# Performance work log

Hardware: AMD Instinct MI355X
Metric: run time of the kernel (lower is better)

The kernel has to match this reference:

```python
import jax, jax.numpy as jnp
import numpy as np

THRESHOLD = 0.5     # overlap_thresh
NEG_POS = 3         # negative:positive ratio
VAR = (0.1, 0.2)    # cfg['variance']


def point_form(pr):
    # cxcywh -> xmin,ymin,xmax,ymax
    return jnp.concatenate([pr[:, :2] - pr[:, 2:] / 2, pr[:, :2] + pr[:, 2:] / 2], axis=1)


def jaccard(a, b):
    # a: [N,4] point-form truths, b: [P,4] point-form priors -> IoU [N,P]
    lt = jnp.maximum(a[:, None, :2], b[None, :, :2])
    rb = jnp.minimum(a[:, None, 2:], b[None, :, 2:])
    wh = jnp.clip(rb - lt, 0.0)
    inter = wh[..., 0] * wh[..., 1]
    area_a = ((a[:, 2] - a[:, 0]) * (a[:, 3] - a[:, 1]))[:, None]
    area_b = ((b[:, 2] - b[:, 0]) * (b[:, 3] - b[:, 1]))[None, :]
    return inter / (area_a + area_b - inter)


def encode(matched, priors):
    # matched: [P,4] point-form, priors: [P,4] cxcywh
    g_cxcy = ((matched[:, :2] + matched[:, 2:]) / 2 - priors[:, :2]) / (VAR[0] * priors[:, 2:])
    g_wh = jnp.log((matched[:, 2:] - matched[:, :2]) / priors[:, 2:]) / VAR[1]
    return jnp.concatenate([g_cxcy, g_wh], axis=1)


def match_one(truths, labels, priors):
    # truths [N,4], labels [N], priors [P,4] cxcywh
    N = truths.shape[0]
    P = priors.shape[0]
    overlaps = jaccard(truths, point_form(priors))          # [N,P]
    best_prior_idx = jnp.argmax(overlaps, axis=1)           # [N] best prior per truth
    best_truth_overlap = jnp.max(overlaps, axis=0)          # [P]
    best_truth_idx = jnp.argmax(overlaps, axis=0)           # [P]
    # ensure each truth's best prior is kept (overlap forced to 2)
    best_truth_overlap = best_truth_overlap.at[best_prior_idx].set(2.0)
    hit = best_prior_idx[:, None] == jnp.arange(P)[None, :]  # [N,P]
    chosen = jnp.max(jnp.where(hit, jnp.arange(N)[:, None], -1), axis=0)
    best_truth_idx = jnp.where(chosen >= 0, chosen, best_truth_idx)
    matched = truths[best_truth_idx]                        # [P,4]
    conf = labels[best_truth_idx].astype(jnp.int32) + 1
    conf = jnp.where(best_truth_overlap < THRESHOLD, 0, conf)
    return encode(matched, priors), conf


def smooth_l1(x):
    ax = jnp.abs(x)
    return jnp.where(ax < 1.0, 0.5 * ax * ax, ax - 0.5)


def multibox_loss(loc_data, conf_data, priors, targets):
    num, P, C = conf_data.shape
    truths = targets[..., :4]
    labels = targets[..., 4]
    loc_t, conf_t = jax.vmap(match_one, in_axes=(0, 0, None))(truths, labels, priors)
    pos = conf_t > 0                                        # [B,P]

    # localization loss over positives
    loss_l = jnp.sum(jnp.where(pos[..., None], smooth_l1(loc_data - loc_t), 0.0))

    # hard-negative mining score: logsumexp - conf[label clamped to {0,1}]
    batch_conf = jax.lax.stop_gradient(conf_data).reshape(-1, C)
    conf_flat = conf_t.reshape(-1)
    clamped = jnp.where(conf_flat != 0, 1, conf_flat)
    # replicate torch nonzero()-indexing quirk: row 0 also set to 1 if any positive exists
    clamped = clamped.at[0].set(jnp.where(jnp.any(conf_flat != 0), 1, clamped[0]))
    lse = jax.scipy.special.logsumexp(batch_conf, axis=1)
    loss_c = lse - jnp.take_along_axis(batch_conf, clamped[:, None], axis=1)[:, 0]
    loss_c = loss_c.reshape(num, P)
    loss_c = jnp.where(pos, 0.0, loss_c)
    # rank of each prior by descending mining loss
    idx_rank = jnp.argsort(jnp.argsort(-loss_c, axis=1), axis=1)
    num_pos = jnp.sum(pos.astype(jnp.int32), axis=1, keepdims=True)  # [B,1]
    num_neg = jnp.clip(NEG_POS * num_pos, None, P - 1)
    neg = idx_rank < num_neg
    sel = pos | neg

    # confidence cross-entropy over selected priors, original labels as targets
    logp = jax.nn.log_softmax(conf_data, axis=-1)           # [B,P,C]
    ce = -jnp.take_along_axis(logp, conf_t[..., None], axis=-1)[..., 0]
    loss_conf = jnp.sum(jnp.where(sel, ce, 0.0))

    Nf = jnp.sum(num_pos).astype(jnp.float32)
    return loss_l / Nf, loss_conf / Nf


def setup_inputs() -> dict:
    key = jax.random.key(0)
    k1, k2, k3, k4, k5, k6, k7 = jax.random.split(key, 7)
    B, P, C, NOBJ = 128, 8732, 21, 20
    loc_data = jax.random.normal(k1, (B, P, 4), jnp.float32)
    conf_data = jax.random.normal(k2, (B, P, C), jnp.float32)
    pcxy = jax.random.uniform(k3, (P, 2), jnp.float32, 0.05, 0.95)
    pwh = jax.random.uniform(k4, (P, 2), jnp.float32, 0.05, 0.4)
    priors = jnp.concatenate([pcxy, pwh], axis=1)           # cxcywh
    mins = jax.random.uniform(k5, (B, NOBJ, 2), jnp.float32, 0.0, 0.6)
    wh = jax.random.uniform(k6, (B, NOBJ, 2), jnp.float32, 0.05, 0.35)
    lab = jax.random.randint(k7, (B, NOBJ), 0, C - 1).astype(jnp.float32)
    targets = jnp.concatenate([mins, mins + wh, lab[..., None]], axis=-1)
    return {"loc_data": loc_data, "conf_data": conf_data, "priors": priors, "targets": targets}


def reference(loc_data, conf_data, priors, targets):
    return multibox_loss(loc_data, conf_data, priors, targets)
```

## Files before the change

kernel.cpp:

```cpp
#include <hip/hip_runtime.h>

#define PP 8732
#define NB 20
#define NC 21
#define BTH 256
#define NCH 35
#define BTS 1024
#define NWS (BTS/64)

__device__ __forceinline__ float sl1(float d){
  float a = fabsf(d);
  return a < 1.0f ? 0.5f*a*a : a - 0.5f;
}

__device__ __forceinline__ float wave_max64(float x){
  int t;
  t = __builtin_amdgcn_update_dpp(0, __float_as_int(x), 0x111, 0xF, 0xF, true); x = fmaxf(x, __int_as_float(t));
  t = __builtin_amdgcn_update_dpp(0, __float_as_int(x), 0x112, 0xF, 0xF, true); x = fmaxf(x, __int_as_float(t));
  t = __builtin_amdgcn_update_dpp(0, __float_as_int(x), 0x114, 0xF, 0xF, true); x = fmaxf(x, __int_as_float(t));
  t = __builtin_amdgcn_update_dpp(0, __float_as_int(x), 0x118, 0xF, 0xF, true); x = fmaxf(x, __int_as_float(t));
  t = __builtin_amdgcn_update_dpp(0, __float_as_int(x), 0x142, 0xF, 0xF, true); x = fmaxf(x, __int_as_float(t));
  t = __builtin_amdgcn_update_dpp(0, __float_as_int(x), 0x143, 0xF, 0xF, true); x = fmaxf(x, __int_as_float(t));
  return __int_as_float(__builtin_amdgcn_readlane(__float_as_int(x), 63));
}

__device__ __forceinline__ int wave_sum64_lane63(int x){
  x += __builtin_amdgcn_update_dpp(0, x, 0x111, 0xF, 0xF, true);
  x += __builtin_amdgcn_update_dpp(0, x, 0x112, 0xF, 0xF, true);
  x += __builtin_amdgcn_update_dpp(0, x, 0x114, 0xF, 0xF, true);
  x += __builtin_amdgcn_update_dpp(0, x, 0x118, 0xF, 0xF, true);
  x += __builtin_amdgcn_update_dpp(0, x, 0x142, 0xF, 0xF, true);
  x += __builtin_amdgcn_update_dpp(0, x, 0x143, 0xF, 0xF, true);
  return x;
}

extern "C" __global__ void __launch_bounds__(BTH)
mb_main(const float* __restrict__ conf_data,
        const float* __restrict__ priors,
        const float* __restrict__ targets,
        float* __restrict__ rankneg,
        unsigned char* __restrict__ meta,
        unsigned long long* __restrict__ keys2)
{
  const int b = blockIdx.x, chunk = blockIdx.y;
  const int tid = threadIdx.x, lane = tid & 63, wid = tid >> 6;
  const int q0 = chunk*BTH + wid*64;
  const int cnt = (q0 < PP) ? ((PP - q0 < 64) ? (PP - q0) : 64) : 0;

  __shared__ __align__(16) float s_buf[4][64*NC];
  __shared__ unsigned long long s_keys[4][NB];

  const bool valid = (lane < cnt);
  const int p  = q0 + lane;
  const int pl = valid ? p : 0;

  float tx=0.f, ty=0.f, tz=0.f, tw=0.f;
  if (lane < NB){
    const float* tp = targets + ((long)b*NB + lane)*5;
    tx = tp[0]; ty = tp[1]; tz = tp[2]; tw = tp[3];
  }
  float4 pr = reinterpret_cast<const float4*>(priors)[pl];

  if (cnt == 64){
    const char* g = (const char*)(conf_data + ((long)b*PP + q0)*NC) + lane*16;
    char* l0 = (char*)&s_buf[wid][0];
    #pragma unroll
    for (int i=0;i<5;i++)
      __builtin_amdgcn_global_load_lds(
        (const __attribute__((address_space(1))) void*)(g + i*1024),
        (__attribute__((address_space(3))) void*)(l0 + i*1024), 16, 0, 0);
    if (lane < 16)
      __builtin_amdgcn_global_load_lds(
        (const __attribute__((address_space(1))) void*)(g + 5*1024),
        (__attribute__((address_space(3))) void*)(l0 + 5*1024), 16, 0, 0);
  } else if (cnt > 0){
    const float4* cb4 = reinterpret_cast<const float4*>(conf_data + ((long)b*PP + q0)*NC);
    float4* sb4 = reinterpret_cast<float4*>(s_buf[wid]);
    const int tot4 = (cnt*NC) >> 2;
    for (int i=lane; i<tot4; i+=64) sb4[i] = cb4[i];
  }

  float bx1 = pr.x - pr.z*0.5f, by1 = pr.y - pr.w*0.5f;
  float bx2 = pr.x + pr.z*0.5f, by2 = pr.y + pr.w*0.5f;
  float area_b = (bx2-bx1)*(by2-by1);
  float area_a = (tz-tx)*(tw-ty);
  float bestov = -1.0f; int bestn = 0;
  unsigned long long mykey = 0ULL;

  if (cnt > 0){
    #pragma unroll 4
    for (int n=0;n<NB;n++){
      float t_x = __int_as_float(__builtin_amdgcn_readlane(__float_as_int(tx), n));
      float t_y = __int_as_float(__builtin_amdgcn_readlane(__float_as_int(ty), n));
      float t_z = __int_as_float(__builtin_amdgcn_readlane(__float_as_int(tz), n));
      float t_w = __int_as_float(__builtin_amdgcn_readlane(__float_as_int(tw), n));
      float aa  = __int_as_float(__builtin_amdgcn_readlane(__float_as_int(area_a), n));
      float lx=fmaxf(t_x,bx1), ly=fmaxf(t_y,by1);
      float rx=fminf(t_z,bx2), ry=fminf(t_w,by2);
      float iw=fmaxf(rx-lx,0.f), ih=fmaxf(ry-ly,0.f);
      float inter = iw*ih;
      float iou = inter * __builtin_amdgcn_rcpf(aa + area_b - inter);
      if (iou > bestov){ bestov=iou; bestn=n; }

      float iouv = valid ? iou : -1.0f;
      float wmax = wave_max64(iouv);
      unsigned long long mk = __ballot(valid && (iou == wmax));
      int wlane = __ffsll((long long)mk) - 1;
      unsigned long long key = ((unsigned long long)__float_as_uint(wmax)<<32)
                             | (unsigned long long)(0xFFFFFFFFu - (unsigned)(q0 + wlane));
      if (lane == n) mykey = key;
    }
  }
  if (lane < NB) s_keys[wid][lane] = mykey;

  if (cnt > 0){
    asm volatile("s_waitcnt vmcnt(0)" ::: "memory");

    const float* v = s_buf[wid] + lane*NC;
    float vv[NC];
    #pragma unroll
    for (int c=0;c<NC;c++) vv[c] = v[c];
    float m = vv[0];
    #pragma unroll
    for (int c=1;c<NC;c++) m = fmaxf(m, vv[c]);
    float s = 0.f;
    #pragma unroll
    for (int c=0;c<NC;c++) s += __expf(vv[c]-m);
    float lse = __logf(s) + m;
    if (valid){
      rankneg[(long)b*PP + p] = lse - vv[0];
      meta[(long)b*PP + p] = (unsigned char)((bestn<<1) | (bestov >= 0.5f ? 1 : 0));
    }
  }

  __syncthreads();
  if (tid < NB){
    unsigned long long mx = s_keys[0][tid];
    #pragma unroll
    for (int w=1;w<4;w++) if (s_keys[w][tid] > mx) mx = s_keys[w][tid];
    keys2[((long)b*NCH + chunk)*NB + tid] = mx;
  }
}

extern "C" __global__ void __launch_bounds__(BTS)
mb_select(const float* __restrict__ loc_data,
          const float* __restrict__ conf_data,
          const float* __restrict__ priors,
          const float* __restrict__ targets,
          const float* __restrict__ rankneg,
          const unsigned char* __restrict__ meta,
          const unsigned long long* __restrict__ keys2,
          float* __restrict__ rowres, int* __restrict__ ticket,
          float* __restrict__ out, int Bn)
{
  const int b = blockIdx.x, tid = threadIdx.x, lane = tid & 63, wid = tid >> 6;
  __shared__ __align__(16) float s_val[PP];
  __shared__ __align__(16) unsigned int s_meta4[PP/4];
  __shared__ float4 s_tr4[NB];
  __shared__ float s_lab[NB];
  __shared__ int   s_bp[NB];
  __shared__ int   s_tot[32];
  __shared__ float s_fa[NWS], s_fb[NWS], s_fc[NWS];
  __shared__ int   s_ia[NWS];
  __shared__ float s_rowll, s_rowpc;
  __shared__ int   s_npos, s_last;
  unsigned char* s_meta = (unsigned char*)s_meta4;
  float4* sv4 = reinterpret_cast<float4*>(s_val);

  const float4* rr = reinterpret_cast<const float4*>(rankneg + (long)b*PP);
  for (int i=tid;i<PP/4;i+=BTS) sv4[i]=rr[i];
  const unsigned int* mr = reinterpret_cast<const unsigned int*>(meta + (long)b*PP);
  for (int i=tid;i<PP/4;i+=BTS) s_meta4[i]=mr[i];
  if (tid < NB*5){
    int n = tid/5, k2 = tid-n*5;
    float vv = targets[((long)b*NB+n)*5+k2];
    if (k2<4) ((float*)&s_tr4[n])[k2]=vv; else s_lab[n]=vv;
  }
  if (tid < NB){
    unsigned long long mx = 0ULL;
    #pragma unroll
    for (int c=0;c<NCH;c++){
      unsigned long long kk = keys2[((long)b*NCH + c)*NB + tid];
      if (kk > mx) mx = kk;
    }
    s_bp[tid] = (int)(0xFFFFFFFFu - (unsigned)(mx & 0xFFFFFFFFULL));
  }
  if (tid < 32) s_tot[tid] = 0;
  __syncthreads();

  if (tid==0){
    for (int n=0;n<NB;n++) s_meta[s_bp[n]] = (unsigned char)((n<<1)|1);
  }
  __syncthreads();

  float4 rv0 = sv4[tid];
  float4 rv1 = sv4[tid+1024];
  float4 rv2 = (tid < PP/4-2048) ? sv4[tid+2048]
                                 : make_float4(0.f,0.f,0.f,0.f);
  unsigned mm0 = s_meta4[tid];
  unsigned mm1 = s_meta4[tid+1024];
  unsigned mm2 = (tid < PP/4-2048) ? s_meta4[tid+2048] : 0u;
  if (mm0 & 0x00000001u) rv0.x = 0.f;
  if (mm0 & 0x00000100u) rv0.y = 0.f;
  if (mm0 & 0x00010000u) rv0.z = 0.f;
  if (mm0 & 0x01000000u) rv0.w = 0.f;
  if (mm1 & 0x00000001u) rv1.x = 0.f;
  if (mm1 & 0x00000100u) rv1.y = 0.f;
  if (mm1 & 0x00010000u) rv1.z = 0.f;
  if (mm1 & 0x01000000u) rv1.w = 0.f;
  if (mm2 & 0x00000001u) rv2.x = 0.f;
  if (mm2 & 0x00000100u) rv2.y = 0.f;
  if (mm2 & 0x00010000u) rv2.z = 0.f;
  if (mm2 & 0x01000000u) rv2.w = 0.f;

  int spec = 0; float delta = 0.f, val0 = 0.f;
  if (b==0 && tid==0 && !(mm0 & 1u)){
    float v0 = conf_data[0], v1 = conf_data[1];
    float r0 = rv0.x;
    float r0p = r0 + v0 - v1;
    delta = r0 - r0p;
    spec = 1;
    rv0.x = r0p; val0 = r0p;
  }

  float ll=0.f, pc=0.f; int np=0;
  for (int p=tid;p<PP;p+=BTS){
    int mt = s_meta[p];
    if (mt & 1){
      np++;
      int n = mt>>1;
      int ct = (int)s_lab[n] + 1;
      const float* cp = conf_data + ((long)b*PP+p)*NC;
      float v0 = cp[0], vct = cp[ct];
      pc += s_val[p] + v0 - vct;
      float4 t = s_tr4[n];
      float4 prr = reinterpret_cast<const float4*>(priors)[p];
      float4 ld = reinterpret_cast<const float4*>(loc_data)[(long)b*PP+p];
      float g0 = ((t.x+t.z)*0.5f - prr.x)/(0.1f*prr.z);
      float g1 = ((t.y+t.w)*0.5f - prr.y)/(0.1f*prr.w);
      float g2 = __logf((t.z-t.x)/prr.z)/0.2f;
      float g3 = __logf((t.w-t.y)/prr.w)/0.2f;
      ll += sl1(ld.x-g0)+sl1(ld.y-g1)+sl1(ld.z-g2)+sl1(ld.w-g3);
    }
  }
  #pragma unroll
  for (int o=32;o;o>>=1){
    ll += __shfl_down(ll,o,64);
    pc += __shfl_down(pc,o,64);
    np += __shfl_down(np,o,64);
  }
  if (lane==0){ s_fa[wid]=ll; s_fb[wid]=pc; s_ia[wid]=np; }
  __syncthreads();
  if (tid==0){
    float a=0.f,c2=0.f; int ni=0;
    for (int w=0;w<NWS;w++){ a+=s_fa[w]; c2+=s_fb[w]; ni+=s_ia[w]; }
    s_rowll=a; s_rowpc=c2; s_npos=ni;
  }
  __syncthreads();
  const int num_pos = s_npos;
  int k = num_pos*3; if (k > PP-1) k = PP-1;

  float negsum = 0.f;
  if (k > 0){
    unsigned lo=0u, hi=0x7f800000u;
    int it=0;
    while (lo < hi){
      unsigned mid = lo + ((hi - lo + 1u) >> 1);
      int c = (__float_as_uint(rv0.x)>=mid) + (__float_as_uint(rv0.y)>=mid)
            + (__float_as_uint(rv0.z)>=mid) + (__float_as_uint(rv0.w)>=mid)
            + (__float_as_uint(rv1.x)>=mid) + (__float_as_uint(rv1.y)>=mid)
            + (__float_as_uint(rv1.z)>=mid) + (__float_as_uint(rv1.w)>=mid)
            + (__float_as_uint(rv2.x)>=mid) + (__float_as_uint(rv2.y)>=mid)
            + (__float_as_uint(rv2.z)>=mid) + (__float_as_uint(rv2.w)>=mid);
      c = wave_sum64_lane63(c);
      if (lane==63) atomicAdd(&s_tot[it], c);
      __syncthreads();
      int tot = s_tot[it];
      if (tot >= k) lo = mid; else hi = mid - 1u;
      it++;
    }
    const unsigned vstar = lo;

    int cg=0; float sg=0.f;
    #define ACC(x) if (__float_as_uint(x)>vstar){cg++;sg+=(x);}
    ACC(rv0.x) ACC(rv0.y) ACC(rv0.z) ACC(rv0.w)
    ACC(rv1.x) ACC(rv1.y) ACC(rv1.z) ACC(rv1.w)
    ACC(rv2.x) ACC(rv2.y) ACC(rv2.z) ACC(rv2.w)
    #undef ACC
    #pragma unroll
    for (int o=32;o;o>>=1){ cg += __shfl_down(cg,o,64); sg += __shfl_down(sg,o,64); }
    __syncthreads();
    if (lane==0){ s_ia[wid]=cg; s_fa[wid]=sg; }
    __syncthreads();
    if (tid==0){
      int cG=0; float sumG=0.f;
      for (int w=0;w<NWS;w++){ cG+=s_ia[w]; sumG+=s_fa[w]; }
      int tie = k - cG;
      negsum = sumG + (float)tie * __uint_as_float(vstar);
      if (b==0 && spec && __float_as_uint(val0) >= vstar) negsum += delta;
    }
  }

  if (tid==0){
    rowres[b*4+0] = s_rowll;
    rowres[b*4+1] = s_rowpc + negsum;
    rowres[b*4+2] = (float)num_pos;
    __threadfence();
    int t = atomicAdd(ticket, 1);
    s_last = (t == gridDim.x - 1) ? 1 : 0;
  }
  __syncthreads();

  if (s_last){
    __threadfence();
    float a0=0.f, a1=0.f, a2=0.f;
    for (int i=tid;i<Bn;i+=BTS){
      a0 += rowres[i*4+0]; a1 += rowres[i*4+1]; a2 += rowres[i*4+2];
    }
    #pragma unroll
    for (int o=32;o;o>>=1){
      a0 += __shfl_down(a0,o,64);
      a1 += __shfl_down(a1,o,64);
      a2 += __shfl_down(a2,o,64);
    }
    if (lane==0){ s_fa[wid]=a0; s_fb[wid]=a1; s_fc[wid]=a2; }
    __syncthreads();
    if (tid==0){
      float A0=0.f,A1=0.f,A2=0.f;
      for (int w=0;w<NWS;w++){ A0+=s_fa[w]; A1+=s_fb[w]; A2+=s_fc[w]; }
      out[0] = A0/A2;
      out[1] = A1/A2;
    }
  }
}

extern "C" void kernel_launch(void* const* d_in, const int* in_sizes, int n_in,
                              void* d_out, int out_size, void* d_ws, size_t ws_size,
                              hipStream_t stream) {
  const float* loc     = (const float*)d_in[0];
  const float* conf    = (const float*)d_in[1];
  const float* priors  = (const float*)d_in[2];
  const float* targets = (const float*)d_in[3];
  float* out = (float*)d_out;
  int B = in_sizes[0] / (PP*4);

  char* ws = (char*)d_ws;
  int*   ticket = (int*)ws;
  float* rowres = (float*)(ws + 64);
  unsigned long long* keys2 = (unsigned long long*)(ws + 4096);
  size_t off_rank = 4096 + (size_t)B*NCH*NB*8;
  float* rankneg = (float*)(ws + off_rank);
  unsigned char* metaa = (unsigned char*)(ws + off_rank + (size_t)B*PP*4);

  hipMemsetAsync(d_ws, 0, 64, stream);
  hipLaunchKernelGGL(mb_main,   dim3(B, NCH), dim3(BTH), 0, stream,
                     conf, priors, targets, rankneg, metaa, keys2);
  hipLaunchKernelGGL(mb_select, dim3(B), dim3(BTS), 0, stream,
                     loc, conf, priors, targets, rankneg, metaa, keys2,
                     rowres, ticket, out, B);
}
```

Before: 202.1 us.

## Fuse main and select kernels using per-row last-block ticket

Merges the two kernels into one launch with 1024-thread blocks over 9 chunks per row. The last chunk block to finish each row, detected through a per-row atomic counter, runs the hard-negative selection and loss reduction, which removes the second launch and its tail. Confidence rows are now loaded directly into registers as float4 instead of through LDS async copies, and rankneg is read from global memory instead of being staged in shared memory. In exchange, only one block per row does the selection work while the other blocks exit, and the larger blocks may lower occupancy in the first phase.

```diff
diff --git a/kernel.cpp b/kernel.cpp
--- a/kernel.cpp
+++ b/kernel.cpp
@@ -3,10 +3,9 @@
 #define PP 8732
 #define NB 20
 #define NC 21
-#define BTH 256
-#define NCH 35
 #define BTS 1024
-#define NWS (BTS/64)
+#define NWS 16
+#define NCH 9
 
 __device__ __forceinline__ float sl1(float d){
   float a = fabsf(d);
@@ -34,60 +33,60 @@
   return x;
 }
 
-extern "C" __global__ void __launch_bounds__(BTH)
-mb_main(const float* __restrict__ conf_data,
-        const float* __restrict__ priors,
-        const float* __restrict__ targets,
-        float* __restrict__ rankneg,
-        unsigned char* __restrict__ meta,
-        unsigned long long* __restrict__ keys2)
+extern "C" __global__ void __launch_bounds__(BTS)
+mb_fused(const float* __restrict__ loc_data,
+         const float* __restrict__ conf_data,
+         const float* __restrict__ priors,
+         const float* __restrict__ targets,
+         float* __restrict__ rankneg,
+         unsigned char* __restrict__ meta,
+         unsigned long long* __restrict__ keys2,
+         int* __restrict__ done,
+         float* __restrict__ rowres, int* __restrict__ ticket,
+         float* __restrict__ out, int Bn)
 {
   const int b = blockIdx.x, chunk = blockIdx.y;
   const int tid = threadIdx.x, lane = tid & 63, wid = tid >> 6;
-  const int q0 = chunk*BTH + wid*64;
+  const int q0 = chunk*BTS + wid*64;
   const int cnt = (q0 < PP) ? ((PP - q0 < 64) ? (PP - q0) : 64) : 0;
 
-  __shared__ __align__(16) float s_buf[4][64*NC];
-  __shared__ unsigned long long s_keys[4][NB];
-
-  const bool valid = (lane < cnt);
-  const int p  = q0 + lane;
-  const int pl = valid ? p : 0;
-
-  float tx=0.f, ty=0.f, tz=0.f, tw=0.f;
-  if (lane < NB){
-    const float* tp = targets + ((long)b*NB + lane)*5;
-    tx = tp[0]; ty = tp[1]; tz = tp[2]; tw = tp[3];
-  }
-  float4 pr = reinterpret_cast<const float4*>(priors)[pl];
-
-  if (cnt == 64){
-    const char* g = (const char*)(conf_data + ((long)b*PP + q0)*NC) + lane*16;
-    char* l0 = (char*)&s_buf[wid][0];
-    #pragma unroll
-    for (int i=0;i<5;i++)
-      __builtin_amdgcn_global_load_lds(
-        (const __attribute__((address_space(1))) void*)(g + i*1024),
-        (__attribute__((address_space(3))) void*)(l0 + i*1024), 16, 0, 0);
-    if (lane < 16)
-      __builtin_amdgcn_global_load_lds(
-        (const __attribute__((address_space(1))) void*)(g + 5*1024),
-        (__attribute__((address_space(3))) void*)(l0 + 5*1024), 16, 0, 0);
-  } else if (cnt > 0){
-    const float4* cb4 = reinterpret_cast<const float4*>(conf_data + ((long)b*PP + q0)*NC);
-    float4* sb4 = reinterpret_cast<float4*>(s_buf[wid]);
-    const int tot4 = (cnt*NC) >> 2;
-    for (int i=lane; i<tot4; i+=64) sb4[i] = cb4[i];
-  }
-
-  float bx1 = pr.x - pr.z*0.5f, by1 = pr.y - pr.w*0.5f;
-  float bx2 = pr.x + pr.z*0.5f, by2 = pr.y + pr.w*0.5f;
-  float area_b = (bx2-bx1)*(by2-by1);
-  float area_a = (tz-tx)*(tw-ty);
-  float bestov = -1.0f; int bestn = 0;
+  __shared__ unsigned long long s_keys[NWS][NB];
+  __shared__ __align__(16) unsigned int s_meta4[PP/4];
+  __shared__ float4 s_tr4[NB];
+  __shared__ float s_lab[NB];
+  __shared__ int   s_bp[NB];
+  __shared__ int   s_tot[32];
+  __shared__ float s_fa[NWS], s_fb[NWS], s_fc[NWS];
+  __shared__ int   s_ia[NWS];
+  __shared__ float s_rowll, s_rowpc;
+  __shared__ int   s_npos, s_go, s_last;
+  unsigned char* s_meta = (unsigned char*)s_meta4;
+
   unsigned long long mykey = 0ULL;
 
   if (cnt > 0){
+    const bool valid = (lane < cnt);
+    const int p  = q0 + lane;
+    const int pl = valid ? p : q0;
+
+    float tx=0.f, ty=0.f, tz=0.f, tw=0.f;
+    if (lane < NB){
+      const float* tp = targets + ((long)b*NB + lane)*5;
+      tx = tp[0]; ty = tp[1]; tz = tp[2]; tw = tp[3];
+    }
+    float4 pr = reinterpret_cast<const float4*>(priors)[pl];
+
+    const float* cb = conf_data + ((long)b*PP + pl)*NC;
+    const float4* cb4 = reinterpret_cast<const float4*>(cb);
+    float4 ca0 = cb4[0], ca1 = cb4[1], ca2 = cb4[2], ca3 = cb4[3], ca4 = cb4[4];
+    float c20 = cb[20];
+
+    float bx1 = pr.x - pr.z*0.5f, by1 = pr.y - pr.w*0.5f;
+    float bx2 = pr.x + pr.z*0.5f, by2 = pr.y + pr.w*0.5f;
+    float area_b = (bx2-bx1)*(by2-by1);
+    float area_a = (tz-tx)*(tw-ty);
+    float bestov = -1.0f; int bestn = 0;
+
     #pragma unroll 4
     for (int n=0;n<NB;n++){
       float t_x = __int_as_float(__builtin_amdgcn_readlane(__float_as_int(tx), n));
@@ -110,16 +109,10 @@
                              | (unsigned long long)(0xFFFFFFFFu - (unsigned)(q0 + wlane));
       if (lane == n) mykey = key;
     }
-  }
-  if (lane < NB) s_keys[wid][lane] = mykey;
-
-  if (cnt > 0){
-    asm volatile("s_waitcnt vmcnt(0)" ::: "memory");
-
-    const float* v = s_buf[wid] + lane*NC;
-    float vv[NC];
-    #pragma unroll
-    for (int c=0;c<NC;c++) vv[c] = v[c];
+
+    float vv[NC] = {ca0.x,ca0.y,ca0.z,ca0.w, ca1.x,ca1.y,ca1.z,ca1.w,
+                    ca2.x,ca2.y,ca2.z,ca2.w, ca3.x,ca3.y,ca3.z,ca3.w,
+                    ca4.x,ca4.y,ca4.z,ca4.w, c20};
     float m = vv[0];
     #pragma unroll
     for (int c=1;c<NC;c++) m = fmaxf(m, vv[c]);
@@ -132,49 +125,35 @@
       meta[(long)b*PP + p] = (unsigned char)((bestn<<1) | (bestov >= 0.5f ? 1 : 0));
     }
   }
+  if (lane < NB) s_keys[wid][lane] = mykey;
 
   __syncthreads();
   if (tid < NB){
     unsigned long long mx = s_keys[0][tid];
     #pragma unroll
-    for (int w=1;w<4;w++) if (s_keys[w][tid] > mx) mx = s_keys[w][tid];
+    for (int w=1;w<NWS;w++) if (s_keys[w][tid] > mx) mx = s_keys[w][tid];
     keys2[((long)b*NCH + chunk)*NB + tid] = mx;
   }
-}
-
-extern "C" __global__ void __launch_bounds__(BTS)
-mb_select(const float* __restrict__ loc_data,
-          const float* __restrict__ conf_data,
-          const float* __restrict__ priors,
-          const float* __restrict__ targets,
-          const float* __restrict__ rankneg,
-          const unsigned char* __restrict__ meta,
-          const unsigned long long* __restrict__ keys2,
-          float* __restrict__ rowres, int* __restrict__ ticket,
-          float* __restrict__ out, int Bn)
-{
-  const int b = blockIdx.x, tid = threadIdx.x, lane = tid & 63, wid = tid >> 6;
-  __shared__ __align__(16) float s_val[PP];
-  __shared__ __align__(16) unsigned int s_meta4[PP/4];
-  __shared__ float4 s_tr4[NB];
-  __shared__ float s_lab[NB];
-  __shared__ int   s_bp[NB];
-  __shared__ int   s_tot[32];
-  __shared__ float s_fa[NWS], s_fb[NWS], s_fc[NWS];
-  __shared__ int   s_ia[NWS];
-  __shared__ float s_rowll, s_rowpc;
-  __shared__ int   s_npos, s_last;
-  unsigned char* s_meta = (unsigned char*)s_meta4;
-  float4* sv4 = reinterpret_cast<float4*>(s_val);
+
+  __threadfence();
+  __syncthreads();
+  if (tid == 0) s_go = (atomicAdd(&done[b], 1) == NCH-1) ? 1 : 0;
+  __syncthreads();
+  if (!s_go) return;
+
+  __threadfence();
 
   const float4* rr = reinterpret_cast<const float4*>(rankneg + (long)b*PP);
-  for (int i=tid;i<PP/4;i+=BTS) sv4[i]=rr[i];
+  float4 rv0 = rr[tid];
+  float4 rv1 = rr[tid+1024];
+  float4 rv2 = (tid < PP/4-2048) ? rr[tid+2048] : make_float4(0.f,0.f,0.f,0.f);
+
   const unsigned int* mr = reinterpret_cast<const unsigned int*>(meta + (long)b*PP);
   for (int i=tid;i<PP/4;i+=BTS) s_meta4[i]=mr[i];
   if (tid < NB*5){
     int n = tid/5, k2 = tid-n*5;
-    float vv = targets[((long)b*NB+n)*5+k2];
-    if (k2<4) ((float*)&s_tr4[n])[k2]=vv; else s_lab[n]=vv;
+    float vvv = targets[((long)b*NB+n)*5+k2];
+    if (k2<4) ((float*)&s_tr4[n])[k2]=vvv; else s_lab[n]=vvv;
   }
   if (tid < NB){
     unsigned long long mx = 0ULL;
@@ -193,10 +172,6 @@
   }
   __syncthreads();
 
-  float4 rv0 = sv4[tid];
-  float4 rv1 = sv4[tid+1024];
-  float4 rv2 = (tid < PP/4-2048) ? sv4[tid+2048]
-                                 : make_float4(0.f,0.f,0.f,0.f);
   unsigned mm0 = s_meta4[tid];
   unsigned mm1 = s_meta4[tid+1024];
   unsigned mm2 = (tid < PP/4-2048) ? s_meta4[tid+2048] : 0u;
@@ -232,7 +207,7 @@
       int ct = (int)s_lab[n] + 1;
       const float* cp = conf_data + ((long)b*PP+p)*NC;
       float v0 = cp[0], vct = cp[ct];
-      pc += s_val[p] + v0 - vct;
+      pc += rankneg[(long)b*PP + p] + v0 - vct;
       float4 t = s_tr4[n];
       float4 prr = reinterpret_cast<const float4*>(priors)[p];
       float4 ld = reinterpret_cast<const float4*>(loc_data)[(long)b*PP+p];
@@ -307,7 +282,7 @@
     rowres[b*4+2] = (float)num_pos;
     __threadfence();
     int t = atomicAdd(ticket, 1);
-    s_last = (t == gridDim.x - 1) ? 1 : 0;
+    s_last = (t == Bn - 1) ? 1 : 0;
   }
   __syncthreads();
 
@@ -346,16 +321,16 @@
 
   char* ws = (char*)d_ws;
   int*   ticket = (int*)ws;
-  float* rowres = (float*)(ws + 64);
-  unsigned long long* keys2 = (unsigned long long*)(ws + 4096);
-  size_t off_rank = 4096 + (size_t)B*NCH*NB*8;
+  int*   done   = (int*)(ws + 64);
+  float* rowres = (float*)(ws + 4096);
+  size_t off_keys = 4096 + (size_t)((B*16 + 255) & ~255);
+  unsigned long long* keys2 = (unsigned long long*)(ws + off_keys);
+  size_t off_rank = (off_keys + (size_t)B*NCH*NB*8 + 255) & ~(size_t)255;
   float* rankneg = (float*)(ws + off_rank);
   unsigned char* metaa = (unsigned char*)(ws + off_rank + (size_t)B*PP*4);
 
-  hipMemsetAsync(d_ws, 0, 64, stream);
-  hipLaunchKernelGGL(mb_main,   dim3(B, NCH), dim3(BTH), 0, stream,
-                     conf, priors, targets, rankneg, metaa, keys2);
-  hipLaunchKernelGGL(mb_select, dim3(B), dim3(BTS), 0, stream,
+  hipMemsetAsync(d_ws, 0, 4096, stream);
+  hipLaunchKernelGGL(mb_fused, dim3(B, NCH), dim3(BTS), 0, stream,
                      loc, conf, priors, targets, rankneg, metaa, keys2,
-                     rowres, ticket, out, B);
-}
+                     done, rowres, ticket, out, B);
+}
```

New measurement: 518.4 us. 2.56x slower.

## Fuse matching/log-sum-exp kernel into per-row select kernel using LDS

Applied to the files above, without the earlier changes.

Merges the two-kernel pipeline into one kernel with one 1024-thread block per batch row. Each block loops over the priors in nine passes, computing IoU matching, per-truth best-prior keys and the log-sum-exp confidence term directly into shared memory. This removes the global round trip of the rankneg, meta and keys2 intermediates and one kernel launch. In exchange, the grid shrinks to only B blocks, so parallelism drops sharply. The per-pass conf loads are also waited on without overlapping the next pass, and LDS use rises substantially.

```diff
diff --git a/kernel.cpp b/kernel.cpp
--- a/kernel.cpp
+++ b/kernel.cpp
@@ -3,10 +3,9 @@
 #define PP 8732
 #define NB 20
 #define NC 21
-#define BTH 256
-#define NCH 35
 #define BTS 1024
-#define NWS (BTS/64)
+#define NWS 16
+#define NPASS 9
 
 __device__ __forceinline__ float sl1(float d){
   float a = fabsf(d);
@@ -34,128 +33,20 @@
   return x;
 }
 
-extern "C" __global__ void __launch_bounds__(BTH)
-mb_main(const float* __restrict__ conf_data,
-        const float* __restrict__ priors,
-        const float* __restrict__ targets,
-        float* __restrict__ rankneg,
-        unsigned char* __restrict__ meta,
-        unsigned long long* __restrict__ keys2)
-{
-  const int b = blockIdx.x, chunk = blockIdx.y;
-  const int tid = threadIdx.x, lane = tid & 63, wid = tid >> 6;
-  const int q0 = chunk*BTH + wid*64;
-  const int cnt = (q0 < PP) ? ((PP - q0 < 64) ? (PP - q0) : 64) : 0;
-
-  __shared__ __align__(16) float s_buf[4][64*NC];
-  __shared__ unsigned long long s_keys[4][NB];
-
-  const bool valid = (lane < cnt);
-  const int p  = q0 + lane;
-  const int pl = valid ? p : 0;
-
-  float tx=0.f, ty=0.f, tz=0.f, tw=0.f;
-  if (lane < NB){
-    const float* tp = targets + ((long)b*NB + lane)*5;
-    tx = tp[0]; ty = tp[1]; tz = tp[2]; tw = tp[3];
-  }
-  float4 pr = reinterpret_cast<const float4*>(priors)[pl];
-
-  if (cnt == 64){
-    const char* g = (const char*)(conf_data + ((long)b*PP + q0)*NC) + lane*16;
-    char* l0 = (char*)&s_buf[wid][0];
-    #pragma unroll
-    for (int i=0;i<5;i++)
-      __builtin_amdgcn_global_load_lds(
-        (const __attribute__((address_space(1))) void*)(g + i*1024),
-        (__attribute__((address_space(3))) void*)(l0 + i*1024), 16, 0, 0);
-    if (lane < 16)
-      __builtin_amdgcn_global_load_lds(
-        (const __attribute__((address_space(1))) void*)(g + 5*1024),
-        (__attribute__((address_space(3))) void*)(l0 + 5*1024), 16, 0, 0);
-  } else if (cnt > 0){
-    const float4* cb4 = reinterpret_cast<const float4*>(conf_data + ((long)b*PP + q0)*NC);
-    float4* sb4 = reinterpret_cast<float4*>(s_buf[wid]);
-    const int tot4 = (cnt*NC) >> 2;
-    for (int i=lane; i<tot4; i+=64) sb4[i] = cb4[i];
-  }
-
-  float bx1 = pr.x - pr.z*0.5f, by1 = pr.y - pr.w*0.5f;
-  float bx2 = pr.x + pr.z*0.5f, by2 = pr.y + pr.w*0.5f;
-  float area_b = (bx2-bx1)*(by2-by1);
-  float area_a = (tz-tx)*(tw-ty);
-  float bestov = -1.0f; int bestn = 0;
-  unsigned long long mykey = 0ULL;
-
-  if (cnt > 0){
-    #pragma unroll 4
-    for (int n=0;n<NB;n++){
-      float t_x = __int_as_float(__builtin_amdgcn_readlane(__float_as_int(tx), n));
-      float t_y = __int_as_float(__builtin_amdgcn_readlane(__float_as_int(ty), n));
-      float t_z = __int_as_float(__builtin_amdgcn_readlane(__float_as_int(tz), n));
-      float t_w = __int_as_float(__builtin_amdgcn_readlane(__float_as_int(tw), n));
-      float aa  = __int_as_float(__builtin_amdgcn_readlane(__float_as_int(area_a), n));
-      float lx=fmaxf(t_x,bx1), ly=fmaxf(t_y,by1);
-      float rx=fminf(t_z,bx2), ry=fminf(t_w,by2);
-      float iw=fmaxf(rx-lx,0.f), ih=fmaxf(ry-ly,0.f);
-      float inter = iw*ih;
-      float iou = inter * __builtin_amdgcn_rcpf(aa + area_b - inter);
-      if (iou > bestov){ bestov=iou; bestn=n; }
-
-      float iouv = valid ? iou : -1.0f;
-      float wmax = wave_max64(iouv);
-      unsigned long long mk = __ballot(valid && (iou == wmax));
-      int wlane = __ffsll((long long)mk) - 1;
-      unsigned long long key = ((unsigned long long)__float_as_uint(wmax)<<32)
-                             | (unsigned long long)(0xFFFFFFFFu - (unsigned)(q0 + wlane));
-      if (lane == n) mykey = key;
-    }
-  }
-  if (lane < NB) s_keys[wid][lane] = mykey;
-
-  if (cnt > 0){
-    asm volatile("s_waitcnt vmcnt(0)" ::: "memory");
-
-    const float* v = s_buf[wid] + lane*NC;
-    float vv[NC];
-    #pragma unroll
-    for (int c=0;c<NC;c++) vv[c] = v[c];
-    float m = vv[0];
-    #pragma unroll
-    for (int c=1;c<NC;c++) m = fmaxf(m, vv[c]);
-    float s = 0.f;
-    #pragma unroll
-    for (int c=0;c<NC;c++) s += __expf(vv[c]-m);
-    float lse = __logf(s) + m;
-    if (valid){
-      rankneg[(long)b*PP + p] = lse - vv[0];
-      meta[(long)b*PP + p] = (unsigned char)((bestn<<1) | (bestov >= 0.5f ? 1 : 0));
-    }
-  }
-
-  __syncthreads();
-  if (tid < NB){
-    unsigned long long mx = s_keys[0][tid];
-    #pragma unroll
-    for (int w=1;w<4;w++) if (s_keys[w][tid] > mx) mx = s_keys[w][tid];
-    keys2[((long)b*NCH + chunk)*NB + tid] = mx;
-  }
-}
-
 extern "C" __global__ void __launch_bounds__(BTS)
-mb_select(const float* __restrict__ loc_data,
-          const float* __restrict__ conf_data,
-          const float* __restrict__ priors,
-          const float* __restrict__ targets,
-          const float* __restrict__ rankneg,
-          const unsigned char* __restrict__ meta,
-          const unsigned long long* __restrict__ keys2,
-          float* __restrict__ rowres, int* __restrict__ ticket,
-          float* __restrict__ out, int Bn)
+mb_row(const float* __restrict__ loc_data,
+       const float* __restrict__ conf_data,
+       const float* __restrict__ priors,
+       const float* __restrict__ targets,
+       float* __restrict__ rowres, int* __restrict__ ticket,
+       float* __restrict__ out, int Bn)
 {
   const int b = blockIdx.x, tid = threadIdx.x, lane = tid & 63, wid = tid >> 6;
+
+  __shared__ __align__(16) float s_buf[NWS][64*NC];
   __shared__ __align__(16) float s_val[PP];
   __shared__ __align__(16) unsigned int s_meta4[PP/4];
+  __shared__ unsigned long long s_keys[NWS][NB];
   __shared__ float4 s_tr4[NB];
   __shared__ float s_lab[NB];
   __shared__ int   s_bp[NB];
@@ -167,25 +58,109 @@
   unsigned char* s_meta = (unsigned char*)s_meta4;
   float4* sv4 = reinterpret_cast<float4*>(s_val);
 
-  const float4* rr = reinterpret_cast<const float4*>(rankneg + (long)b*PP);
-  for (int i=tid;i<PP/4;i+=BTS) sv4[i]=rr[i];
-  const unsigned int* mr = reinterpret_cast<const unsigned int*>(meta + (long)b*PP);
-  for (int i=tid;i<PP/4;i+=BTS) s_meta4[i]=mr[i];
   if (tid < NB*5){
     int n = tid/5, k2 = tid-n*5;
-    float vv = targets[((long)b*NB+n)*5+k2];
-    if (k2<4) ((float*)&s_tr4[n])[k2]=vv; else s_lab[n]=vv;
-  }
+    float vvv = targets[((long)b*NB+n)*5+k2];
+    if (k2<4) ((float*)&s_tr4[n])[k2]=vvv; else s_lab[n]=vvv;
+  }
+  if (tid < 32) s_tot[tid] = 0;
+
+  float tx=0.f, ty=0.f, tz=0.f, tw=0.f;
+  if (lane < NB){
+    const float* tp = targets + ((long)b*NB + lane)*5;
+    tx = tp[0]; ty = tp[1]; tz = tp[2]; tw = tp[3];
+  }
+  const float area_a = (tz-tx)*(tw-ty);
+
+  unsigned long long mykey = 0ULL;
+
+  for (int pass=0; pass<NPASS; ++pass){
+    const int q0 = pass*BTS + wid*64;
+    const int cnt = (q0 < PP) ? ((PP - q0 < 64) ? (PP - q0) : 64) : 0;
+
+    if (cnt == 64){
+      asm volatile("s_waitcnt lgkmcnt(0)" ::: "memory");
+      const char* g = (const char*)(conf_data + ((long)b*PP + q0)*NC) + lane*16;
+      char* l0 = (char*)&s_buf[wid][0];
+      #pragma unroll
+      for (int i=0;i<5;i++)
+        __builtin_amdgcn_global_load_lds(
+          (const __attribute__((address_space(1))) void*)(g + i*1024),
+          (__attribute__((address_space(3))) void*)(l0 + i*1024), 16, 0, 0);
+      if (lane < 16)
+        __builtin_amdgcn_global_load_lds(
+          (const __attribute__((address_space(1))) void*)(g + 5*1024),
+          (__attribute__((address_space(3))) void*)(l0 + 5*1024), 16, 0, 0);
+    } else if (cnt > 0){
+      asm volatile("s_waitcnt lgkmcnt(0)" ::: "memory");
+      const float4* cb4 = reinterpret_cast<const float4*>(conf_data + ((long)b*PP + q0)*NC);
+      float4* sb4 = reinterpret_cast<float4*>(s_buf[wid]);
+      const int tot4 = (cnt*NC) >> 2;
+      for (int i=lane; i<tot4; i+=64) sb4[i] = cb4[i];
+    }
+
+    if (cnt > 0){
+      const bool valid = (lane < cnt);
+      const int p  = q0 + lane;
+      const int pl = valid ? p : q0;
+      float4 pr = reinterpret_cast<const float4*>(priors)[pl];
+
+      float bx1 = pr.x - pr.z*0.5f, by1 = pr.y - pr.w*0.5f;
+      float bx2 = pr.x + pr.z*0.5f, by2 = pr.y + pr.w*0.5f;
+      float area_b = (bx2-bx1)*(by2-by1);
+      float bestov = -1.0f; int bestn = 0;
+
+      #pragma unroll 4
+      for (int n=0;n<NB;n++){
+        float t_x = __int_as_float(__builtin_amdgcn_readlane(__float_as_int(tx), n));
+        float t_y = __int_as_float(__builtin_amdgcn_readlane(__float_as_int(ty), n));
+        float t_z = __int_as_float(__builtin_amdgcn_readlane(__float_as_int(tz), n));
+        float t_w = __int_as_float(__builtin_amdgcn_readlane(__float_as_int(tw), n));
+        float aa  = __int_as_float(__builtin_amdgcn_readlane(__float_as_int(area_a), n));
+        float lx=fmaxf(t_x,bx1), ly=fmaxf(t_y,by1);
+        float rx=fminf(t_z,bx2), ry=fminf(t_w,by2);
+        float iw=fmaxf(rx-lx,0.f), ih=fmaxf(ry-ly,0.f);
+        float inter = iw*ih;
+        float iou = inter * __builtin_amdgcn_rcpf(aa + area_b - inter);
+        if (iou > bestov){ bestov=iou; bestn=n; }
+
+        float iouv = valid ? iou : -1.0f;
+        float wmax = wave_max64(iouv);
+        unsigned long long mk = __ballot(valid && (iou == wmax));
+        int wlane = __ffsll((long long)mk) - 1;
+        unsigned long long key = ((unsigned long long)__float_as_uint(wmax)<<32)
+                               | (unsigned long long)(0xFFFFFFFFu - (unsigned)(q0 + wlane));
+        if (lane == n && key > mykey) mykey = key;
+      }
+
+      asm volatile("s_waitcnt vmcnt(0)" ::: "memory");
+
+      const float* v = s_buf[wid] + lane*NC;
+      float vv[NC];
+      #pragma unroll
+      for (int c=0;c<NC;c++) vv[c] = v[c];
+      float m = vv[0];
+      #pragma unroll
+      for (int c=1;c<NC;c++) m = fmaxf(m, vv[c]);
+      float s = 0.f;
+      #pragma unroll
+      for (int c=0;c<NC;c++) s += __expf(vv[c]-m);
+      float lse = __logf(s) + m;
+      if (valid){
+        s_val[p]  = lse - vv[0];
+        s_meta[p] = (unsigned char)((bestn<<1) | (bestov >= 0.5f ? 1 : 0));
+      }
+    }
+  }
+  if (lane < NB) s_keys[wid][lane] = mykey;
+  __syncthreads();
+
   if (tid < NB){
-    unsigned long long mx = 0ULL;
+    unsigned long long mx = s_keys[0][tid];
     #pragma unroll
-    for (int c=0;c<NCH;c++){
-      unsigned long long kk = keys2[((long)b*NCH + c)*NB + tid];
-      if (kk > mx) mx = kk;
-    }
+    for (int w=1;w<NWS;w++) if (s_keys[w][tid] > mx) mx = s_keys[w][tid];
     s_bp[tid] = (int)(0xFFFFFFFFu - (unsigned)(mx & 0xFFFFFFFFULL));
   }
-  if (tid < 32) s_tot[tid] = 0;
   __syncthreads();
 
   if (tid==0){
@@ -195,8 +170,7 @@
 
   float4 rv0 = sv4[tid];
   float4 rv1 = sv4[tid+1024];
-  float4 rv2 = (tid < PP/4-2048) ? sv4[tid+2048]
-                                 : make_float4(0.f,0.f,0.f,0.f);
+  float4 rv2 = (tid < PP/4-2048) ? sv4[tid+2048] : make_float4(0.f,0.f,0.f,0.f);
   unsigned mm0 = s_meta4[tid];
   unsigned mm1 = s_meta4[tid+1024];
   unsigned mm2 = (tid < PP/4-2048) ? s_meta4[tid+2048] : 0u;
@@ -307,7 +281,7 @@
     rowres[b*4+2] = (float)num_pos;
     __threadfence();
     int t = atomicAdd(ticket, 1);
-    s_last = (t == gridDim.x - 1) ? 1 : 0;
+    s_last = (t == Bn - 1) ? 1 : 0;
   }
   __syncthreads();
 
@@ -346,16 +320,9 @@
 
   char* ws = (char*)d_ws;
   int*   ticket = (int*)ws;
-  float* rowres = (float*)(ws + 64);
-  unsigned long long* keys2 = (unsigned long long*)(ws + 4096);
-  size_t off_rank = 4096 + (size_t)B*NCH*NB*8;
-  float* rankneg = (float*)(ws + off_rank);
-  unsigned char* metaa = (unsigned char*)(ws + off_rank + (size_t)B*PP*4);
+  float* rowres = (float*)(ws + 4096);
 
   hipMemsetAsync(d_ws, 0, 64, stream);
-  hipLaunchKernelGGL(mb_main,   dim3(B, NCH), dim3(BTH), 0, stream,
-                     conf, priors, targets, rankneg, metaa, keys2);
-  hipLaunchKernelGGL(mb_select, dim3(B), dim3(BTS), 0, stream,
-                     loc, conf, priors, targets, rankneg, metaa, keys2,
-                     rowres, ticket, out, B);
-}
+  hipLaunchKernelGGL(mb_row, dim3(B), dim3(BTS), 0, stream,
+                     loc, conf, priors, targets, rowres, ticket, out, B);
+}
```

After: 237.1 us. 1.17x slower.

## Process four priors per thread in mb_main to amortize wave reductions

Applied to the files above, without the earlier changes.

Each thread now handles four consecutive priors instead of one, so each block covers 1024 priors and the chunk count drops from 35 to 9. Truth boxes are staged in shared memory instead of being broadcast with readlane. The per-truth wave max and ballot are now paid once per four priors, and rankneg/meta are stored as vectorized float4 and packed bytes. The conf row is loaded straight into registers with float4 loads, replacing the async global-to-LDS copy. This trades the coalesced LDS staging for strided 84-byte per-thread loads, raises register pressure, and leaves fewer blocks to fill the GPU.

```diff
diff --git a/kernel.cpp b/kernel.cpp
--- a/kernel.cpp
+++ b/kernel.cpp
@@ -4,7 +4,7 @@
 #define NB 20
 #define NC 21
 #define BTH 256
-#define NCH 35
+#define NCH 9
 #define BTS 1024
 #define NWS (BTS/64)
 
@@ -44,95 +44,108 @@
 {
   const int b = blockIdx.x, chunk = blockIdx.y;
   const int tid = threadIdx.x, lane = tid & 63, wid = tid >> 6;
-  const int q0 = chunk*BTH + wid*64;
-  const int cnt = (q0 < PP) ? ((PP - q0 < 64) ? (PP - q0) : 64) : 0;
-
-  __shared__ __align__(16) float s_buf[4][64*NC];
+  const int q0w = chunk*1024 + wid*256;
+  const int p0  = q0w + 4*lane;
+
+  __shared__ float4 s_tr4[NB];
+  __shared__ float  s_area[NB];
   __shared__ unsigned long long s_keys[4][NB];
 
-  const bool valid = (lane < cnt);
-  const int p  = q0 + lane;
-  const int pl = valid ? p : 0;
-
-  float tx=0.f, ty=0.f, tz=0.f, tw=0.f;
-  if (lane < NB){
-    const float* tp = targets + ((long)b*NB + lane)*5;
-    tx = tp[0]; ty = tp[1]; tz = tp[2]; tw = tp[3];
-  }
-  float4 pr = reinterpret_cast<const float4*>(priors)[pl];
-
-  if (cnt == 64){
-    const char* g = (const char*)(conf_data + ((long)b*PP + q0)*NC) + lane*16;
-    char* l0 = (char*)&s_buf[wid][0];
-    #pragma unroll
-    for (int i=0;i<5;i++)
-      __builtin_amdgcn_global_load_lds(
-        (const __attribute__((address_space(1))) void*)(g + i*1024),
-        (__attribute__((address_space(3))) void*)(l0 + i*1024), 16, 0, 0);
-    if (lane < 16)
-      __builtin_amdgcn_global_load_lds(
-        (const __attribute__((address_space(1))) void*)(g + 5*1024),
-        (__attribute__((address_space(3))) void*)(l0 + 5*1024), 16, 0, 0);
-  } else if (cnt > 0){
-    const float4* cb4 = reinterpret_cast<const float4*>(conf_data + ((long)b*PP + q0)*NC);
-    float4* sb4 = reinterpret_cast<float4*>(s_buf[wid]);
-    const int tot4 = (cnt*NC) >> 2;
-    for (int i=lane; i<tot4; i+=64) sb4[i] = cb4[i];
-  }
-
-  float bx1 = pr.x - pr.z*0.5f, by1 = pr.y - pr.w*0.5f;
-  float bx2 = pr.x + pr.z*0.5f, by2 = pr.y + pr.w*0.5f;
-  float area_b = (bx2-bx1)*(by2-by1);
-  float area_a = (tz-tx)*(tw-ty);
-  float bestov = -1.0f; int bestn = 0;
+  if (tid < NB){
+    const float* tp = targets + ((long)b*NB + tid)*5;
+    float a0=tp[0], a1=tp[1], a2=tp[2], a3=tp[3];
+    s_tr4[tid]  = make_float4(a0,a1,a2,a3);
+    s_area[tid] = (a2-a0)*(a3-a1);
+  }
+  __syncthreads();
+
   unsigned long long mykey = 0ULL;
 
-  if (cnt > 0){
+  if (q0w < PP){
+    const bool fullwave = (q0w + 256 <= PP);
+
+    float bx1[4], by1[4], bx2[4], by2[4], areab[4];
+    #pragma unroll
+    for (int i=0;i<4;i++){
+      int p = p0 + i;
+      int pc = (p < PP) ? p : 0;
+      float4 pr = reinterpret_cast<const float4*>(priors)[pc];
+      float x1 = pr.x - pr.z*0.5f, y1 = pr.y - pr.w*0.5f;
+      float x2 = pr.x + pr.z*0.5f, y2 = pr.y + pr.w*0.5f;
+      if (!fullwave && p >= PP){ x1=3e9f; y1=3e9f; x2=3e9f; y2=3e9f; }
+      bx1[i]=x1; by1[i]=y1; bx2[i]=x2; by2[i]=y2;
+      areab[i] = (x2-x1)*(y2-y1);
+    }
+
+    float bestov[4] = {-1.f,-1.f,-1.f,-1.f};
+    int   bestn [4] = {0,0,0,0};
+
     #pragma unroll 4
     for (int n=0;n<NB;n++){
-      float t_x = __int_as_float(__builtin_amdgcn_readlane(__float_as_int(tx), n));
-      float t_y = __int_as_float(__builtin_amdgcn_readlane(__float_as_int(ty), n));
-      float t_z = __int_as_float(__builtin_amdgcn_readlane(__float_as_int(tz), n));
-      float t_w = __int_as_float(__builtin_amdgcn_readlane(__float_as_int(tw), n));
-      float aa  = __int_as_float(__builtin_amdgcn_readlane(__float_as_int(area_a), n));
-      float lx=fmaxf(t_x,bx1), ly=fmaxf(t_y,by1);
-      float rx=fminf(t_z,bx2), ry=fminf(t_w,by2);
-      float iw=fmaxf(rx-lx,0.f), ih=fmaxf(ry-ly,0.f);
-      float inter = iw*ih;
-      float iou = inter * __builtin_amdgcn_rcpf(aa + area_b - inter);
-      if (iou > bestov){ bestov=iou; bestn=n; }
-
-      float iouv = valid ? iou : -1.0f;
-      float wmax = wave_max64(iouv);
-      unsigned long long mk = __ballot(valid && (iou == wmax));
+      float4 t = s_tr4[n];
+      float aa = s_area[n];
+      float candiou = -1.0f; unsigned candp = 0u;
+      #pragma unroll
+      for (int i=0;i<4;i++){
+        float lx=fmaxf(t.x,bx1[i]), ly=fmaxf(t.y,by1[i]);
+        float rx=fminf(t.z,bx2[i]), ry=fminf(t.w,by2[i]);
+        float iw=fmaxf(rx-lx,0.f), ih=fmaxf(ry-ly,0.f);
+        float inter = iw*ih;
+        float iou = inter * __builtin_amdgcn_rcpf(aa + areab[i] - inter);
+        if (iou > bestov[i]){ bestov[i]=iou; bestn[i]=n; }
+        if (iou > candiou){ candiou=iou; candp=(unsigned)(p0+i); }
+      }
+      float wmax = wave_max64(candiou);
+      unsigned long long mk = __ballot(candiou == wmax);
       int wlane = __ffsll((long long)mk) - 1;
+      unsigned wp = (unsigned)__builtin_amdgcn_readlane((int)candp, wlane);
       unsigned long long key = ((unsigned long long)__float_as_uint(wmax)<<32)
-                             | (unsigned long long)(0xFFFFFFFFu - (unsigned)(q0 + wlane));
+                             | (unsigned long long)(0xFFFFFFFFu - wp);
       if (lane == n) mykey = key;
     }
-  }
+
+    float rr4[4] = {0.f,0.f,0.f,0.f};
+    unsigned metab = 0u;
+    #pragma unroll
+    for (int i=0;i<4;i++){
+      int p = p0 + i;
+      if (p < PP){
+        const float* cb = conf_data + ((long)b*PP + p)*NC;
+        const float4* cb4 = reinterpret_cast<const float4*>(cb);
+        float4 ca0=cb4[0], ca1=cb4[1], ca2=cb4[2], ca3=cb4[3], ca4=cb4[4];
+        float c20 = cb[20];
+        float vv[NC] = {ca0.x,ca0.y,ca0.z,ca0.w, ca1.x,ca1.y,ca1.z,ca1.w,
+                        ca2.x,ca2.y,ca2.z,ca2.w, ca3.x,ca3.y,ca3.z,ca3.w,
+                        ca4.x,ca4.y,ca4.z,ca4.w, c20};
+        float m = vv[0];
+        #pragma unroll
+        for (int c=1;c<NC;c++) m = fmaxf(m, vv[c]);
+        float s = 0.f;
+        #pragma unroll
+        for (int c=0;c<NC;c++) s += __expf(vv[c]-m);
+        float lse = __logf(s) + m;
+        rr4[i] = lse - vv[0];
+        metab |= ((unsigned)((bestn[i]<<1) | (bestov[i] >= 0.5f ? 1 : 0))) << (8*i);
+      }
+    }
+
+    if (p0 + 3 < PP){
+      *reinterpret_cast<float4*>(rankneg + (long)b*PP + p0) =
+          make_float4(rr4[0],rr4[1],rr4[2],rr4[3]);
+      *reinterpret_cast<unsigned*>(meta + (long)b*PP + p0) = metab;
+    } else {
+      #pragma unroll
+      for (int i=0;i<4;i++){
+        int p = p0 + i;
+        if (p < PP){
+          rankneg[(long)b*PP + p] = rr4[i];
+          meta[(long)b*PP + p] = (unsigned char)((metab >> (8*i)) & 0xFF);
+        }
+      }
+    }
+  }
+
   if (lane < NB) s_keys[wid][lane] = mykey;
-
-  if (cnt > 0){
-    asm volatile("s_waitcnt vmcnt(0)" ::: "memory");
-
-    const float* v = s_buf[wid] + lane*NC;
-    float vv[NC];
-    #pragma unroll
-    for (int c=0;c<NC;c++) vv[c] = v[c];
-    float m = vv[0];
-    #pragma unroll
-    for (int c=1;c<NC;c++) m = fmaxf(m, vv[c]);
-    float s = 0.f;
-    #pragma unroll
-    for (int c=0;c<NC;c++) s += __expf(vv[c]-m);
-    float lse = __logf(s) + m;
-    if (valid){
-      rankneg[(long)b*PP + p] = lse - vv[0];
-      meta[(long)b*PP + p] = (unsigned char)((bestn<<1) | (bestov >= 0.5f ? 1 : 0));
-    }
-  }
-
   __syncthreads();
   if (tid < NB){
     unsigned long long mx = s_keys[0][tid];
@@ -195,8 +208,7 @@
 
   float4 rv0 = sv4[tid];
   float4 rv1 = sv4[tid+1024];
-  float4 rv2 = (tid < PP/4-2048) ? sv4[tid+2048]
-                                 : make_float4(0.f,0.f,0.f,0.f);
+  float4 rv2 = (tid < PP/4-2048) ? sv4[tid+2048] : make_float4(0.f,0.f,0.f,0.f);
   unsigned mm0 = s_meta4[tid];
   unsigned mm1 = s_meta4[tid+1024];
   unsigned mm2 = (tid < PP/4-2048) ? s_meta4[tid+2048] : 0u;
@@ -307,7 +319,7 @@
     rowres[b*4+2] = (float)num_pos;
     __threadfence();
     int t = atomicAdd(ticket, 1);
-    s_last = (t == gridDim.x - 1) ? 1 : 0;
+    s_last = (t == Bn - 1) ? 1 : 0;
   }
   __syncthreads();
 
```

Result: slower. 206.3 us (+2.1%).
